# Kernel tuning notes

Hardware: AMD Instinct MI355X
Metric: run time of the kernel (lower is better)

The kernel has to match this reference:

```python
import jax, jax.numpy as jnp
import numpy as np
import math

EMBED_DIM = 2048
NUM_HEADS = 16
DEPTH = 12
HEAD_DIM = EMBED_DIM // NUM_HEADS // 2  # 64
LAMBDA_INIT = 0.8 - 0.6 * math.exp(-0.3 * DEPTH)


def setup_inputs() -> dict:
    key = jax.random.key(0)
    ks = jax.random.split(key, 9)
    B, T, E = 2, 2048, EMBED_DIM
    s = 1.0 / math.sqrt(E)
    return {
        "query": jax.random.normal(ks[0], (B, T, E), jnp.float32),
        "Wq": jax.random.normal(ks[1], (E, E), jnp.float32) * s,
        "Wk": jax.random.normal(ks[2], (E, E), jnp.float32) * s,
        "Wv": jax.random.normal(ks[3], (E, E), jnp.float32) * s,
        "Wo": jax.random.normal(ks[4], (E, E), jnp.float32) * s,
        "lambda_q1": jax.random.normal(ks[5], (HEAD_DIM,), jnp.float32) * 0.1,
        "lambda_k1": jax.random.normal(ks[6], (HEAD_DIM,), jnp.float32) * 0.1,
        "lambda_q2": jax.random.normal(ks[7], (HEAD_DIM,), jnp.float32) * 0.1,
        "lambda_k2": jax.random.normal(ks[8], (HEAD_DIM,), jnp.float32) * 0.1,
        "subln_weight": jnp.ones((2 * HEAD_DIM,), jnp.float32),
    }


def _diff_attn(query, Wq, Wk, Wv, Wo, lq1, lk1, lq2, lk2, g):
    B, T, E = query.shape
    H, D = NUM_HEADS, HEAD_DIM
    S = T  # self-attention: key = value = query
    scaling = D ** -0.5

    # projections (nn.Linear: x @ W.T)
    q = (query @ Wq.T).reshape(B, T, 2 * H, D).transpose(0, 2, 1, 3)  # [B,2H,T,D]
    k = (query @ Wk.T).reshape(B, S, 2 * H, D).transpose(0, 2, 1, 3)  # [B,2H,S,D]
    v = (query @ Wv.T).reshape(B, S, H, 2 * D).transpose(0, 2, 1, 3)  # [B,H,S,2D]

    q = q * scaling
    attn = jnp.einsum("bhtd,bhsd->bhts", q, k)  # [B,2H,T,S]
    attn = jnp.nan_to_num(attn)
    # default causal mask (offset = S - T = 0)
    causal = jnp.triu(jnp.full((T, S), -jnp.inf, attn.dtype), k=1)
    attn = jax.nn.softmax(attn + causal, axis=-1)

    lam1 = jnp.exp(jnp.sum(lq1 * lk1))
    lam2 = jnp.exp(jnp.sum(lq2 * lk2))
    lam = lam1 - lam2 + LAMBDA_INIT

    attn = attn.reshape(B, H, 2, T, S)
    attn = attn[:, :, 0] - lam * attn[:, :, 1]  # differential combine [B,H,T,S]

    out = jnp.einsum("bhts,bhsd->bhtd", attn, v)  # [B,H,T,2D]
    # RMSNorm over last dim (2D), eps=1e-5, elementwise affine g
    rms = jax.lax.rsqrt(jnp.mean(out * out, axis=-1, keepdims=True) + 1e-5)
    out = out * rms * g
    out = out * (1.0 - LAMBDA_INIT)
    out = out.transpose(0, 2, 1, 3).reshape(B, T, H * 2 * D)
    return out @ Wo.T


def reference(query, Wq, Wk, Wv, Wo, lambda_q1, lambda_k1, lambda_q2, lambda_k2, subln_weight):
    return _diff_attn(query, Wq, Wk, Wv, Wo, lambda_q1, lambda_k1, lambda_q2, lambda_k2, subln_weight)
```

## Files before the change

### kernel.cpp

```cpp
#include <hip/hip_runtime.h>


#define B_SZ   2
#define T_LEN  2048
#define E_DIM  2048
#define M_ROWS 4096
#define NH     16
#define HH     32
#define HD     64
#define VD     128
#define NQT    16
#define QKLD   4096

#define LAMBDA_INIT_F 0.7836057665316239f
#define ONE_MINUS_LI  0.2163942334683761f

typedef __attribute__((ext_vector_type(4))) float          f32x4;
typedef __attribute__((ext_vector_type(8))) short          s16x8;
typedef __attribute__((ext_vector_type(4))) unsigned short u16x4;
typedef __attribute__((ext_vector_type(8))) __bf16         bf16x8;

typedef const __attribute__((address_space(1))) unsigned int* gas_t;
typedef __attribute__((address_space(3))) unsigned int*       las_t;
__device__ __forceinline__ void gl_lds16(const void* g, void* l) {
  __builtin_amdgcn_global_load_lds((gas_t)g, (las_t)l, 16, 0, 0);
}

__device__ __forceinline__ float bf2f(unsigned short h) {
  union { unsigned u; float f; } v; v.u = ((unsigned)h) << 16; return v.f;
}
__device__ __forceinline__ unsigned short f2bf(float f) {
  union { float f; unsigned u; } v; v.f = f;
  return (unsigned short)((v.u + 0x7fffu + ((v.u >> 16) & 1u)) >> 16);
}
__device__ __forceinline__ unsigned fbits(float f) {
  union { float f; unsigned u; } v; v.f = f; return v.u;
}
__device__ __forceinline__ float bits2f(unsigned u) {
  union { unsigned u; float f; } v; v.u = u; return v.f;
}

__global__ __launch_bounds__(256) void cast_bf16(const float* __restrict__ in,
                                                 unsigned short* __restrict__ out,
                                                 int n4, float scale) {
  int i = blockIdx.x * 256 + threadIdx.x;
  const int stride = gridDim.x * 256;
  for (; i < n4; i += stride) {
    f32x4 v = ((const f32x4*)in)[i];
    u16x4 o;
    o[0] = f2bf(v[0] * scale); o[1] = f2bf(v[1] * scale);
    o[2] = f2bf(v[2] * scale); o[3] = f2bf(v[3] * scale);
    ((u16x4*)out)[i] = o;
  }
}

template <int OUT_F32>
__global__ __launch_bounds__(256) void gemm_bt(const unsigned short* __restrict__ A,
                                               const unsigned short* __restrict__ Bm,
                                               void* __restrict__ Cout,
                                               int M, int N, int K, float alpha) {
  __shared__ unsigned short As[128 * 64];
  __shared__ unsigned short Bs[128 * 64];
  const int tid  = threadIdx.x;
  const int lane = tid & 63;
  const int wave = tid >> 6;
  const int wr = wave >> 1, wc = wave & 1;
  const int lrow = lane & 15, lkb = lane >> 4;
  const int m0 = blockIdx.x * 128, n0 = blockIdx.y * 128;

  f32x4 acc[4][4] = {};

  for (int k0 = 0; k0 < K; k0 += 64) {
#pragma unroll
    for (int it = 0; it < 4; ++it) {
      const int ci  = tid + it * 256;
      const int row = ci >> 3;
      const int cs  = (ci & 7) ^ (row & 7);
      const int rb  = (wave * 64 + it * 256) * 8;
      gl_lds16(A  + (size_t)(m0 + row) * K + k0 + cs * 8, &As[rb]);
      gl_lds16(Bm + (size_t)(n0 + row) * K + k0 + cs * 8, &Bs[rb]);
    }
    __syncthreads();
    bf16x8 af[4][2], bfr[4][2];
#pragma unroll
    for (int mi = 0; mi < 4; ++mi) {
      const int r = wr * 64 + mi * 16 + lrow;
#pragma unroll
      for (int kc = 0; kc < 2; ++kc)
        af[mi][kc] = *(const bf16x8*)(&As[r * 64 + (((kc * 4 + lkb) ^ (r & 7)) * 8)]);
    }
#pragma unroll
    for (int ni = 0; ni < 4; ++ni) {
      const int r = wc * 64 + ni * 16 + lrow;
#pragma unroll
      for (int kc = 0; kc < 2; ++kc)
        bfr[ni][kc] = *(const bf16x8*)(&Bs[r * 64 + (((kc * 4 + lkb) ^ (r & 7)) * 8)]);
    }
#pragma unroll
    for (int mi = 0; mi < 4; ++mi)
#pragma unroll
      for (int ni = 0; ni < 4; ++ni)
#pragma unroll
        for (int kc = 0; kc < 2; ++kc)
          acc[mi][ni] = __builtin_amdgcn_mfma_f32_16x16x32_bf16(af[mi][kc], bfr[ni][kc],
                                                                acc[mi][ni], 0, 0, 0);
    __syncthreads();
  }
#pragma unroll
  for (int mi = 0; mi < 4; ++mi) {
#pragma unroll
    for (int ni = 0; ni < 4; ++ni) {
      const int mb = m0 + wr * 64 + mi * 16 + lkb * 4;
      const int nn = n0 + wc * 64 + ni * 16 + lrow;
#pragma unroll
      for (int r = 0; r < 4; ++r) {
        const float v = acc[mi][ni][r] * alpha;
        const size_t idx = (size_t)(mb + r) * N + nn;
        if (OUT_F32) ((float*)Cout)[idx] = v;
        else         ((unsigned short*)Cout)[idx] = f2bf(v);
      }
    }
  }
}

__device__ __forceinline__ void stage_kv(const unsigned short* __restrict__ Kbase,
                                         const unsigned short* __restrict__ Vbase,
                                         int s0, unsigned short* KsBuf,
                                         unsigned short* VtBuf, int tid, int wave) {
#pragma unroll
  for (int j = 0; j < 2; ++j) {
    const int ci = tid + j * 256;
    const int s = ci >> 3;
    const int cs = (ci & 7) ^ (s & 7);
    gl_lds16(Kbase + (size_t)(s0 + s) * QKLD + cs * 8, KsBuf + (wave * 64 + j * 256) * 8);
  }
#pragma unroll
  for (int cc = 0; cc < 4; ++cc) {
    const int ci = tid + cc * 256;
    const int d = ci >> 3;
    const int cs = (ci & 7) ^ (d & 7);
    gl_lds16(Vbase + (size_t)d * M_ROWS + s0 + cs * 8, VtBuf + (wave * 64 + cc * 256) * 8);
  }
}

__global__ __launch_bounds__(256, 2) void flash_attn_mfma(
    const unsigned short* __restrict__ QK,
    const unsigned short* __restrict__ VT,
    float* __restrict__ Ohalf) {
  const int pr = blockIdx.x;
  const int hh = blockIdx.y;
  const int b  = blockIdx.z;
  const int tid = threadIdx.x, lane = tid & 63, wave = tid >> 6;
  const int g = lane >> 4, lr = lane & 15;
  const int h = hh >> 1;
  const size_t bT = (size_t)b * T_LEN;

  __shared__ unsigned short Ks[2][64 * 64];
  __shared__ unsigned short Vt[2][128 * 64];
  __shared__ unsigned short Pl[128 * 64];

  const unsigned short* Kbase = QK + bT * QKLD + E_DIM + hh * HD;
  const unsigned short* Vbase = VT + (size_t)(h * VD) * M_ROWS + b * T_LEN;

#pragma unroll 1
  for (int half = 0; half < 2; ++half) {
    const int qt = half ? (NQT - 1 - pr) : pr;
    const int qbase = qt * 128;
    const int rw0 = qbase + wave * 32;

    bf16x8 qf[2][2];
#pragma unroll
    for (int mi = 0; mi < 2; ++mi)
#pragma unroll
      for (int kc = 0; kc < 2; ++kc) {
        const int row = qbase + wave * 32 + mi * 16 + lr;
        qf[mi][kc] = *(const bf16x8*)(QK + (bT + row) * QKLD + hh * HD + kc * 32 + g * 8);
      }

    f32x4 Oa[2][8];
#pragma unroll
    for (int mi = 0; mi < 2; ++mi)
#pragma unroll
      for (int dv = 0; dv < 8; ++dv) Oa[mi][dv] = (f32x4){0.f, 0.f, 0.f, 0.f};
    float m_run[2][4], l_part[2][4];
#pragma unroll
    for (int mi = 0; mi < 2; ++mi)
#pragma unroll
      for (int r = 0; r < 4; ++r) { m_run[mi][r] = -1e30f; l_part[mi][r] = 0.f; }

    const int nsteps = 2 * qt + 2;
    __syncthreads();
    stage_kv(Kbase, Vbase, 0, Ks[0], Vt[0], tid, wave);
    int cb = 0;

    for (int ti = 0; ti < nsteps; ++ti) {
      const int s0 = ti * 64;
      __syncthreads();
      if (ti + 1 < nsteps)
        stage_kv(Kbase, Vbase, s0 + 64, Ks[cb ^ 1], Vt[cb ^ 1], tid, wave);

      if (s0 <= rw0 + 31) {
        const unsigned short* ks = Ks[cb];
        const unsigned short* vt = Vt[cb];
        bf16x8 kb[4][2];
#pragma unroll
        for (int nj = 0; nj < 4; ++nj)
#pragma unroll
          for (int kc = 0; kc < 2; ++kc) {
            const int srow = nj * 16 + lr;
            kb[nj][kc] = *(const bf16x8*)(&ks[srow * 64 + (((kc * 4 + g) ^ (srow & 7)) * 8)]);
          }
        f32x4 Sa[2][4];
#pragma unroll
        for (int mi = 0; mi < 2; ++mi)
#pragma unroll
          for (int nj = 0; nj < 4; ++nj) {
            f32x4 acc = (f32x4){0.f, 0.f, 0.f, 0.f};
#pragma unroll
            for (int kc = 0; kc < 2; ++kc)
              acc = __builtin_amdgcn_mfma_f32_16x16x32_bf16(qf[mi][kc], kb[nj][kc], acc, 0, 0, 0);
            Sa[mi][nj] = acc;
          }

        const bool needmask = (s0 + 63) > rw0;
        float mx[2][4];
        bool anew = false;
#pragma unroll
        for (int mi = 0; mi < 2; ++mi)
#pragma unroll
          for (int r = 0; r < 4; ++r) {
            const int rowq = rw0 + mi * 16 + g * 4 + r;
            float m0v = -1e30f;
#pragma unroll
            for (int nj = 0; nj < 4; ++nj) {
              float v = Sa[mi][nj][r];
              if (needmask && (s0 + nj * 16 + lr > rowq)) v = -1e30f;
              Sa[mi][nj][r] = v;
              m0v = fmaxf(m0v, v);
            }
            m0v = fmaxf(m0v, __shfl_xor(m0v, 1));
            m0v = fmaxf(m0v, __shfl_xor(m0v, 2));
            m0v = fmaxf(m0v, __shfl_xor(m0v, 4));
            m0v = fmaxf(m0v, __shfl_xor(m0v, 8));
            mx[mi][r] = m0v;
            anew |= (m0v > m_run[mi][r]);
          }

        if (__any(anew)) {
#pragma unroll
          for (int mi = 0; mi < 2; ++mi)
#pragma unroll
            for (int r = 0; r < 4; ++r) {
              const float mn = fmaxf(m_run[mi][r], mx[mi][r]);
              const float rs = __expf(m_run[mi][r] - mn);
              m_run[mi][r] = mn;
              l_part[mi][r] *= rs;
#pragma unroll
              for (int dv = 0; dv < 8; ++dv) Oa[mi][dv][r] *= rs;
            }
        }

#pragma unroll
        for (int mi = 0; mi < 2; ++mi) {
#pragma unroll
          for (int r = 0; r < 4; ++r) {
            const int row = wave * 32 + mi * 16 + g * 4 + r;
            float ps = 0.f;
#pragma unroll
            for (int nj = 0; nj < 4; ++nj) {
              const float p = __expf(Sa[mi][nj][r] - m_run[mi][r]);
              const unsigned u = fbits(p);
              const int chunk = (nj * 2 + (lr >> 3)) ^ (row & 7);
              Pl[row * 64 + chunk * 8 + (lr & 7)] = (unsigned short)(u >> 16);
              ps += bits2f(u & 0xffff0000u);
            }
            l_part[mi][r] += ps;
          }
        }

        bf16x8 pa[2][2];
#pragma unroll
        for (int mi = 0; mi < 2; ++mi)
#pragma unroll
          for (int kc = 0; kc < 2; ++kc) {
            const int row = wave * 32 + mi * 16 + lr;
            pa[mi][kc] = *(const bf16x8*)(&Pl[row * 64 + (((kc * 4 + g) ^ (row & 7)) * 8)]);
          }
#pragma unroll
        for (int dv = 0; dv < 8; ++dv) {
          bf16x8 vb[2];
#pragma unroll
          for (int kc = 0; kc < 2; ++kc) {
            const int d = dv * 16 + lr;
            vb[kc] = *(const bf16x8*)(&vt[d * 64 + (((kc * 4 + g) ^ (d & 7)) * 8)]);
          }
#pragma unroll
          for (int mi = 0; mi < 2; ++mi)
#pragma unroll
            for (int kc = 0; kc < 2; ++kc)
              Oa[mi][dv] = __builtin_amdgcn_mfma_f32_16x16x32_bf16(pa[mi][kc], vb[kc],
                                                                   Oa[mi][dv], 0, 0, 0);
        }
      }
      cb ^= 1;
    }

#pragma unroll
    for (int mi = 0; mi < 2; ++mi)
#pragma unroll
      for (int r = 0; r < 4; ++r) {
        float ls = l_part[mi][r];
        ls += __shfl_xor(ls, 1);
        ls += __shfl_xor(ls, 2);
        ls += __shfl_xor(ls, 4);
        ls += __shfl_xor(ls, 8);
        const float rn = 1.f / ls;
        const int t = qbase + wave * 32 + mi * 16 + g * 4 + r;
        float* orow = Ohalf + ((size_t)(b * HH + hh) * T_LEN + t) * VD;
#pragma unroll
        for (int dv = 0; dv < 8; ++dv)
          orow[dv * 16 + lr] = Oa[mi][dv][r] * rn;
      }
  }
}

__global__ __launch_bounds__(256) void combine_norm(
    const float* __restrict__ Oh,
    const float* __restrict__ lq1, const float* __restrict__ lk1,
    const float* __restrict__ lq2, const float* __restrict__ lk2,
    const float* __restrict__ g,
    unsigned short* __restrict__ Act) {
  const int lane = threadIdx.x & 63;
  const int r = blockIdx.x * 4 + (threadIdx.x >> 6);
  const int hd = r & 15;
  const int t = (r >> 4) & 2047;
  const int b = r >> 15;
  float p1 = lq1[lane] * lk1[lane];
  float p2 = lq2[lane] * lk2[lane];
#pragma unroll
  for (int o = 1; o < 64; o <<= 1) { p1 += __shfl_xor(p1, o); p2 += __shfl_xor(p2, o); }
  const float lam = __expf(p1) - __expf(p2) + LAMBDA_INIT_F;
  const float* o0 = Oh + ((size_t)(b * HH + 2 * hd) * T_LEN + t) * VD;
  const float* o1 = o0 + (size_t)T_LEN * VD;
  const float x0 = o0[lane]      - lam * o1[lane];
  const float x1 = o0[lane + 64] - lam * o1[lane + 64];
  float ss = x0 * x0 + x1 * x1;
#pragma unroll
  for (int o = 1; o < 64; o <<= 1) ss += __shfl_xor(ss, o);
  const float s = rsqrtf(ss * (1.f / 128.f) + 1e-5f) * ONE_MINUS_LI;
  unsigned short* arow = Act + ((size_t)(b * T_LEN + t) * E_DIM + hd * VD);
  arow[lane]      = f2bf(x0 * s * g[lane]);
  arow[lane + 64] = f2bf(x1 * s * g[lane + 64]);
}

extern "C" void kernel_launch(void* const* d_in, const int* in_sizes, int n_in,
                              void* d_out, int out_size, void* d_ws, size_t ws_size,
                              hipStream_t stream) {
  (void)in_sizes; (void)n_in; (void)out_size; (void)ws_size;
  const float* x   = (const float*)d_in[0];
  const float* Wq  = (const float*)d_in[1];
  const float* Wk  = (const float*)d_in[2];
  const float* Wv  = (const float*)d_in[3];
  const float* Wo  = (const float*)d_in[4];
  const float* lq1 = (const float*)d_in[5];
  const float* lk1 = (const float*)d_in[6];
  const float* lq2 = (const float*)d_in[7];
  const float* lk2 = (const float*)d_in[8];
  const float* g   = (const float*)d_in[9];

  char* p = (char*)d_ws;
  unsigned short* XBF = (unsigned short*)p; p += (size_t)M_ROWS * E_DIM * 2;
  unsigned short* WQB = (unsigned short*)p; p += (size_t)E_DIM * E_DIM * 2;
  unsigned short* WKB = (unsigned short*)p; p += (size_t)E_DIM * E_DIM * 2;
  unsigned short* WVB = (unsigned short*)p; p += (size_t)E_DIM * E_DIM * 2;
  unsigned short* WOB = (unsigned short*)p; p += (size_t)E_DIM * E_DIM * 2;
  unsigned short* QKB = (unsigned short*)p; p += (size_t)M_ROWS * QKLD * 2;
  unsigned short* VTB = (unsigned short*)p; p += (size_t)M_ROWS * E_DIM * 2;
  float*          OH  = (float*)p;          p += (size_t)B_SZ * HH * T_LEN * VD * 4;
  unsigned short* ACT = (unsigned short*)p; p += (size_t)M_ROWS * E_DIM * 2;

  cast_bf16<<<2048, 256, 0, stream>>>(x,  XBF, M_ROWS * E_DIM / 4, 1.0f);
  cast_bf16<<<1024, 256, 0, stream>>>(Wq, WQB, E_DIM * E_DIM / 4, 0.125f);
  cast_bf16<<<1024, 256, 0, stream>>>(Wk, WKB, E_DIM * E_DIM / 4, 1.0f);
  cast_bf16<<<1024, 256, 0, stream>>>(Wv, WVB, E_DIM * E_DIM / 4, 1.0f);
  cast_bf16<<<1024, 256, 0, stream>>>(Wo, WOB, E_DIM * E_DIM / 4, 1.0f);

  dim3 gqk(M_ROWS / 128, (2 * E_DIM) / 128);
  gemm_bt<0><<<gqk, 256, 0, stream>>>(XBF, WQB, QKB, M_ROWS, 2 * E_DIM, E_DIM, 1.0f);
  dim3 gt(E_DIM / 128, M_ROWS / 128);
  gemm_bt<0><<<gt, 256, 0, stream>>>(WVB, XBF, VTB, E_DIM, M_ROWS, E_DIM, 1.0f);

  flash_attn_mfma<<<dim3(NQT / 2, HH, B_SZ), 256, 0, stream>>>(QKB, VTB, OH);

  combine_norm<<<B_SZ * T_LEN * NH / 4, 256, 0, stream>>>(OH, lq1, lk1, lq2, lk2, g, ACT);

  dim3 gg(M_ROWS / 128, E_DIM / 128);
  gemm_bt<1><<<gg, 256, 0, stream>>>(ACT, WOB, d_out, M_ROWS, E_DIM, E_DIM, 1.0f);
}
```

Measured before the change: 473.9 us.

## Replace GEMM with 256x256 double-buffered 8-wave pipelined kernel and lazy softmax rescale

Swaps the 128x128 single-buffered GEMM for a 256x256 tile, 512-thread kernel. It double-buffers LDS, splits the tile into quadrants whose next-k loads are issued between MFMA phases, adds grouped block swizzling for L2 reuse, and raises wave priority around the MFMAs. The aim is to hide global-to-LDS latency and raise arithmetic intensity in the projection GEMMs. Separately, the flash-attention kernel now rescales the running max only when it grows by more than 8, skipping rescale work at some risk of reduced numerical headroom. The larger tile also uses 128KB of LDS per block and gives fewer blocks in flight.

```diff
diff --git a/kernel.cpp b/kernel.cpp
--- a/kernel.cpp
+++ b/kernel.cpp
@@ -55,72 +55,118 @@
 }
 
 template <int OUT_F32>
-__global__ __launch_bounds__(256) void gemm_bt(const unsigned short* __restrict__ A,
-                                               const unsigned short* __restrict__ Bm,
-                                               void* __restrict__ Cout,
-                                               int M, int N, int K, float alpha) {
-  __shared__ unsigned short As[128 * 64];
-  __shared__ unsigned short Bs[128 * 64];
-  const int tid  = threadIdx.x;
-  const int lane = tid & 63;
-  const int wave = tid >> 6;
-  const int wr = wave >> 1, wc = wave & 1;
-  const int lrow = lane & 15, lkb = lane >> 4;
-  const int m0 = blockIdx.x * 128, n0 = blockIdx.y * 128;
-
-  f32x4 acc[4][4] = {};
-
-  for (int k0 = 0; k0 < K; k0 += 64) {
-#pragma unroll
-    for (int it = 0; it < 4; ++it) {
-      const int ci  = tid + it * 256;
+__global__ __launch_bounds__(512, 2) void gemm8(const unsigned short* __restrict__ A,
+                                                const unsigned short* __restrict__ Bm,
+                                                void* __restrict__ Cout,
+                                                int M, int N, int K, float alpha,
+                                                int gx) {
+  __shared__ unsigned short AS[2][2][128 * 64];
+  __shared__ unsigned short BS[2][2][128 * 64];
+  const int tid = threadIdx.x, lane = tid & 63, wave = tid >> 6;
+  const int wm = wave >> 2, wn = wave & 3;
+  const int lr = lane & 15, g = lane >> 4;
+  const int nwg = gridDim.x;
+  const int cpx = nwg >> 3;
+  const int bid = blockIdx.x;
+  const int swz = (bid & 7) * cpx + (bid >> 3);
+  const int bx = swz % gx, by = swz / gx;
+  const int m0 = bx * 256, n0 = by * 256;
+
+  f32x4 acc[8][4] = {};
+  const int NT = K >> 6;
+
+  auto stageA = [&](int t, int h) {
+#pragma unroll
+    for (int l = 0; l < 2; ++l) {
+      const int ci = l * 512 + tid;
       const int row = ci >> 3;
-      const int cs  = (ci & 7) ^ (row & 7);
-      const int rb  = (wave * 64 + it * 256) * 8;
-      gl_lds16(A  + (size_t)(m0 + row) * K + k0 + cs * 8, &As[rb]);
-      gl_lds16(Bm + (size_t)(n0 + row) * K + k0 + cs * 8, &Bs[rb]);
+      const int cs = (ci & 7) ^ (row & 7);
+      gl_lds16(A + (size_t)(m0 + h * 128 + row) * K + t * 64 + cs * 8,
+               &AS[t & 1][h][(l * 512 + wave * 64) * 8]);
     }
-    __syncthreads();
-    bf16x8 af[4][2], bfr[4][2];
-#pragma unroll
-    for (int mi = 0; mi < 4; ++mi) {
-      const int r = wr * 64 + mi * 16 + lrow;
-#pragma unroll
-      for (int kc = 0; kc < 2; ++kc)
-        af[mi][kc] = *(const bf16x8*)(&As[r * 64 + (((kc * 4 + lkb) ^ (r & 7)) * 8)]);
+  };
+  auto stageB = [&](int t, int h) {
+#pragma unroll
+    for (int l = 0; l < 2; ++l) {
+      const int ci = l * 512 + tid;
+      const int row = ci >> 3;
+      const int cs = (ci & 7) ^ (row & 7);
+      gl_lds16(Bm + (size_t)(n0 + h * 128 + row) * K + t * 64 + cs * 8,
+               &BS[t & 1][h][(l * 512 + wave * 64) * 8]);
     }
-#pragma unroll
-    for (int ni = 0; ni < 4; ++ni) {
-      const int r = wc * 64 + ni * 16 + lrow;
-#pragma unroll
-      for (int kc = 0; kc < 2; ++kc)
-        bfr[ni][kc] = *(const bf16x8*)(&Bs[r * 64 + (((kc * 4 + lkb) ^ (r & 7)) * 8)]);
-    }
-#pragma unroll
-    for (int mi = 0; mi < 4; ++mi)
-#pragma unroll
-      for (int ni = 0; ni < 4; ++ni)
+  };
+
+  stageA(0, 0); stageB(0, 0); stageA(0, 1); stageB(0, 1);
+  asm volatile("s_waitcnt vmcnt(4)" ::: "memory");
+  __builtin_amdgcn_sched_barrier(0);
+  __builtin_amdgcn_s_barrier();
+
+  for (int t = 0; t < NT; ++t) {
+    const int cur = t & 1;
+    const bool pf = (t + 1 < NT);
+#pragma unroll
+    for (int p = 0; p < 4; ++p) {
+      const int mh = p & 1;
+      const int nh = p >> 1;
+      bf16x8 af[4][2], bfr[2][2];
+#pragma unroll
+      for (int mf = 0; mf < 4; ++mf) {
+        const int r = wm * 64 + mf * 16 + lr;
 #pragma unroll
         for (int kc = 0; kc < 2; ++kc)
-          acc[mi][ni] = __builtin_amdgcn_mfma_f32_16x16x32_bf16(af[mi][kc], bfr[ni][kc],
-                                                                acc[mi][ni], 0, 0, 0);
-    __syncthreads();
-  }
-#pragma unroll
-  for (int mi = 0; mi < 4; ++mi) {
-#pragma unroll
-    for (int ni = 0; ni < 4; ++ni) {
-      const int mb = m0 + wr * 64 + mi * 16 + lkb * 4;
-      const int nn = n0 + wc * 64 + ni * 16 + lrow;
-#pragma unroll
-      for (int r = 0; r < 4; ++r) {
-        const float v = acc[mi][ni][r] * alpha;
-        const size_t idx = (size_t)(mb + r) * N + nn;
-        if (OUT_F32) ((float*)Cout)[idx] = v;
-        else         ((unsigned short*)Cout)[idx] = f2bf(v);
-      }
+          af[mf][kc] = *(const bf16x8*)(&AS[cur][mh][r * 64 + (((kc * 4 + g) ^ (r & 7)) * 8)]);
+      }
+#pragma unroll
+      for (int nf = 0; nf < 2; ++nf) {
+        const int r = wn * 32 + nf * 16 + lr;
+#pragma unroll
+        for (int kc = 0; kc < 2; ++kc)
+          bfr[nf][kc] = *(const bf16x8*)(&BS[cur][nh][r * 64 + (((kc * 4 + g) ^ (r & 7)) * 8)]);
+      }
+      if (pf) {
+        if (p == 0)      stageA(t + 1, 0);
+        else if (p == 1) stageB(t + 1, 0);
+        else if (p == 2) stageA(t + 1, 1);
+        else             stageB(t + 1, 1);
+      }
+      __builtin_amdgcn_s_barrier();
+      __builtin_amdgcn_s_setprio(1);
+#pragma unroll
+      for (int mf = 0; mf < 4; ++mf)
+#pragma unroll
+        for (int nf = 0; nf < 2; ++nf)
+#pragma unroll
+          for (int kc = 0; kc < 2; ++kc)
+            acc[mh * 4 + mf][nh * 2 + nf] =
+                __builtin_amdgcn_mfma_f32_16x16x32_bf16(af[mf][kc], bfr[nf][kc],
+                                                        acc[mh * 4 + mf][nh * 2 + nf],
+                                                        0, 0, 0);
+      __builtin_amdgcn_s_setprio(0);
+      if (p == 2) asm volatile("s_waitcnt vmcnt(6)" ::: "memory");
+      else        asm volatile("s_waitcnt vmcnt(4)" ::: "memory");
+      __builtin_amdgcn_sched_barrier(0);
+      __builtin_amdgcn_s_barrier();
     }
   }
+
+#pragma unroll
+  for (int mh = 0; mh < 2; ++mh)
+#pragma unroll
+    for (int mf = 0; mf < 4; ++mf)
+#pragma unroll
+      for (int nh = 0; nh < 2; ++nh)
+#pragma unroll
+        for (int nf = 0; nf < 2; ++nf) {
+          const int rowb = m0 + mh * 128 + wm * 64 + mf * 16 + g * 4;
+          const int col  = n0 + nh * 128 + wn * 32 + nf * 16 + lr;
+#pragma unroll
+          for (int r = 0; r < 4; ++r) {
+            const float v = acc[mh * 4 + mf][nh * 2 + nf][r] * alpha;
+            const size_t idx = (size_t)(rowb + r) * N + col;
+            if (OUT_F32) ((float*)Cout)[idx] = v;
+            else         ((unsigned short*)Cout)[idx] = f2bf(v);
+          }
+        }
 }
 
 __device__ __forceinline__ void stage_kv(const unsigned short* __restrict__ Kbase,
@@ -243,7 +289,7 @@
             m0v = fmaxf(m0v, __shfl_xor(m0v, 4));
             m0v = fmaxf(m0v, __shfl_xor(m0v, 8));
             mx[mi][r] = m0v;
-            anew |= (m0v > m_run[mi][r]);
+            anew |= (m0v > m_run[mi][r] + 8.0f);
           }
 
         if (__any(anew)) {
@@ -385,15 +431,15 @@
   cast_bf16<<<1024, 256, 0, stream>>>(Wv, WVB, E_DIM * E_DIM / 4, 1.0f);
   cast_bf16<<<1024, 256, 0, stream>>>(Wo, WOB, E_DIM * E_DIM / 4, 1.0f);
 
-  dim3 gqk(M_ROWS / 128, (2 * E_DIM) / 128);
-  gemm_bt<0><<<gqk, 256, 0, stream>>>(XBF, WQB, QKB, M_ROWS, 2 * E_DIM, E_DIM, 1.0f);
-  dim3 gt(E_DIM / 128, M_ROWS / 128);
-  gemm_bt<0><<<gt, 256, 0, stream>>>(WVB, XBF, VTB, E_DIM, M_ROWS, E_DIM, 1.0f);
+  gemm8<0><<<(M_ROWS / 256) * (2 * E_DIM / 256), 512, 0, stream>>>(
+      XBF, WQB, QKB, M_ROWS, 2 * E_DIM, E_DIM, 1.0f, M_ROWS / 256);
+  gemm8<0><<<(E_DIM / 256) * (M_ROWS / 256), 512, 0, stream>>>(
+      WVB, XBF, VTB, E_DIM, M_ROWS, E_DIM, 1.0f, E_DIM / 256);
 
   flash_attn_mfma<<<dim3(NQT / 2, HH, B_SZ), 256, 0, stream>>>(QKB, VTB, OH);
 
   combine_norm<<<B_SZ * T_LEN * NH / 4, 256, 0, stream>>>(OH, lq1, lk1, lq2, lk2, g, ACT);
 
-  dim3 gg(M_ROWS / 128, E_DIM / 128);
-  gemm_bt<1><<<gg, 256, 0, stream>>>(ACT, WOB, d_out, M_ROWS, E_DIM, E_DIM, 1.0f);
-}
+  gemm8<1><<<(M_ROWS / 256) * (E_DIM / 256), 512, 0, stream>>>(
+      ACT, WOB, d_out, M_ROWS, E_DIM, E_DIM, 1.0f, M_ROWS / 256);
+}
```

Result: slower. 485.0 us (+2.4%).
